# Kernel optimization log

Hardware: AMD Instinct MI355X
Metric: run time of the kernel (lower is better)

The kernel has to match this reference:

```python
import jax, jax.numpy as jnp
import numpy as np

B, T, D, R, V = 32, 14, 1024, 4, 8192


def setup_inputs() -> dict:
    key = jax.random.key(0)
    k1, k2, k3, k4, k5 = jax.random.split(key, 5)
    input_embs = jax.random.normal(k1, (B, T, D), dtype=jnp.float32)
    label_ids = jax.random.randint(k2, (B, T), 0, V)
    w_alpha = jax.random.normal(k3, (D, R), dtype=jnp.float32)
    w_beta = jax.random.normal(k4, (D, R), dtype=jnp.float32)
    w_vocab = jax.random.normal(k5, (D, V * R * R), dtype=jnp.float32)
    return {"input_embs": input_embs, "label_ids": label_ids,
            "w_alpha": w_alpha, "w_beta": w_beta, "w_vocab": w_vocab}


def _tt_params(x, w_alpha, w_beta, w_vocab):
    b, t, d = x.shape
    r = w_alpha.shape[1]
    v = w_vocab.shape[1] // (r * r)
    xf = x.reshape(-1, d)
    alpha = jax.nn.sigmoid((xf @ w_alpha).reshape(b, t, r).mean(1)) + 0.001   # (B,R)
    beta = jax.nn.sigmoid((xf @ w_beta).reshape(b, t, r).mean(1)) + 0.001     # (B,R)
    core = jax.nn.sigmoid((xf @ w_vocab).reshape(b, t, r, v, r).mean(1)) * 0.01 + 0.001  # (B,R,V,R)
    return alpha, beta, core


def _chain_matmul(init, mats):
    # init: (B,R,R); mats: (n,B,R,R) -> sequential product init @ mats[0] @ ...
    def step(carry, m):
        return jnp.einsum('bik,bkj->bij', carry, m), None
    out, _ = jax.lax.scan(step, init, mats)
    return out


def reference(input_embs, label_ids, w_alpha, w_beta, w_vocab):
    alpha, beta, core = _tt_params(input_embs, w_alpha, w_beta, w_vocab)
    b, t = label_ids.shape
    # ---- _select: gather core slices at label indices, chain-multiply ----
    sel = core[jnp.arange(b)[:, None], :, label_ids, :]   # (B,T,R,R)
    sel = jnp.swapaxes(sel, 0, 1)                         # (T,B,R,R)
    chain = _chain_matmul(sel[0], sel[1:])                # (B,R,R)
    unnorm = jnp.einsum('bi,bij,bj->b', alpha, chain, beta)
    # ---- normalization: marginalized core multiplied T extra times (T+1 factors, as in source) ----
    cm = core.sum(axis=2)                                 # (B,R,R)
    cm_rep = jnp.broadcast_to(cm, (t,) + cm.shape)        # (T,B,R,R)
    nres = _chain_matmul(cm, cm_rep)                      # (B,R,R)
    norm = jnp.einsum('bi,bij,bj->b', alpha, nres, beta)
    probs = unnorm / norm + 0.001
    loss = -jnp.log(probs)
    return loss.mean()
```

## Files before the change

kernel.cpp:

```cpp
#include <hip/hip_runtime.h>
#include <cstdint>
#include <cstddef>

#define BB 32
#define TT 14
#define DD 1024
#define RR 4
#define VV 8192
#define NCOL (VV*RR*RR)

typedef float f32x16 __attribute__((ext_vector_type(16)));
typedef short short8 __attribute__((ext_vector_type(8)));
typedef unsigned int uint;


__device__ __forceinline__ ushort bf16_rne(float f) {
    uint u = __builtin_bit_cast(uint, f);
    return (ushort)((u + 0x7FFFu + ((u >> 16) & 1u)) >> 16);
}

__global__ __launch_bounds__(256) void k_prep(const float* __restrict__ in,
                                              float* __restrict__ xb,
                                              float* __restrict__ cm) {
    int tid = blockIdx.x * 256 + threadIdx.x;
    int b = tid >> 10, d = tid & 1023;
    float s = 0.f;
    #pragma unroll
    for (int t = 0; t < TT; ++t) s += in[(b * TT + t) * DD + d];
    xb[b * DD + d] = s * (1.0f / TT);
    if (tid < BB * 16) cm[tid] = 0.f;
}

__global__ __launch_bounds__(64) void k_xfrag(const float* __restrict__ xb,
                                              uint4* __restrict__ xfrag) {
    int s = blockIdx.x;
    int l = threadIdx.x;
    int b = l & 31;
    int kb = s * 16 + (l >> 5) * 8;
    uint u[4];
    #pragma unroll
    for (int p = 0; p < 4; ++p) {
        ushort h0 = bf16_rne(xb[b * DD + kb + 2 * p]);
        ushort h1 = bf16_rne(xb[b * DD + kb + 2 * p + 1]);
        u[p] = (uint)h0 | ((uint)h1 << 16);
    }
    xfrag[(s << 6) + l] = make_uint4(u[0], u[1], u[2], u[3]);
}

__global__ __launch_bounds__(256) void k_ab(const float* __restrict__ xb,
                                            const float* __restrict__ wa,
                                            const float* __restrict__ wb,
                                            float* __restrict__ alpha,
                                            float* __restrict__ beta) {
    int wid  = (blockIdx.x * 256 + threadIdx.x) >> 6;
    int lane = threadIdx.x & 63;
    int b = wid >> 3, r = (wid >> 1) & 3, s = wid & 1;
    const float* wm = s ? wb : wa;
    float p = 0.f;
    #pragma unroll
    for (int k = 0; k < 16; ++k) {
        int d = lane + 64 * k;
        p += xb[b * DD + d] * wm[d * RR + r];
    }
    #pragma unroll
    for (int m = 1; m < 64; m <<= 1) p += __shfl_xor(p, m);
    if (lane == 0) {
        float v = 1.0f / (1.0f + __expf(-p)) + 0.001f;
        (s ? beta : alpha)[b * RR + r] = v;
    }
}

#define LOADW(DST, STEP)                                                      \
    _Pragma("unroll")                                                         \
    for (int j = 0; j < 8; ++j)                                               \
        DST[j] = __builtin_nontemporal_load(                                  \
            wp + (size_t)((STEP) * 16 + j) * NCOL);

__device__ __forceinline__ short8 pack_bf16x8(const float* w) {
    uint u[4];
    #pragma unroll
    for (int p = 0; p < 4; ++p) {
        ushort h0 = bf16_rne(w[2 * p]);
        ushort h1 = bf16_rne(w[2 * p + 1]);
        u[p] = (uint)h0 | ((uint)h1 << 16);
    }
    return __builtin_bit_cast(short8, make_uint4(u[0], u[1], u[2], u[3]));
}

__global__ __launch_bounds__(256) void k_core(const float* __restrict__ wv,
                                              const uint4* __restrict__ xfrag,
                                              const int*   __restrict__ lab,
                                              float* __restrict__ cm,
                                              float* __restrict__ sel) {
    const int tid  = threadIdx.x;
    const int lane = tid & 63;
    const int wvid = tid >> 6;
    const int n0   = blockIdx.x * 128 + wvid * 32;
    const int n    = n0 + (lane & 31);
    const int ii   = n >> 15;
    const int jj   = n & 3;
    const int vv   = (n >> 2) & (VV - 1);

    __shared__ int   lds_lab[BB * TT];
    __shared__ float cm_blk[BB][4];

    for (int idx = tid; idx < BB * TT; idx += 256) lds_lab[idx] = lab[idx];
    if (tid < BB * 4) ((float*)cm_blk)[tid] = 0.f;
    __syncthreads();

    const float* wp = wv + (size_t)((lane >> 5) * 8) * NCOL + n;

    f32x16 acc;
    #pragma unroll
    for (int q = 0; q < 16; ++q) acc[q] = 0.f;

    float wrA[8], wrB[8];
    uint4 axA, axB;
    LOADW(wrA, 0);
    axA = xfrag[lane];

    #pragma unroll 1
    for (int s = 0; s < 64; s += 2) {
        LOADW(wrB, s + 1);
        axB = xfrag[((s + 1) << 6) + lane];
        acc = __builtin_amdgcn_mfma_f32_32x32x16_bf16(
                  __builtin_bit_cast(short8, axA), pack_bf16x8(wrA), acc, 0, 0, 0);
        if (s + 2 < 64) {
            LOADW(wrA, s + 2);
            axA = xfrag[((s + 2) << 6) + lane];
        }
        acc = __builtin_amdgcn_mfma_f32_32x32x16_bf16(
                  __builtin_bit_cast(short8, axB), pack_bf16x8(wrB), acc, 0, 0, 0);
    }

    #pragma unroll
    for (int r = 0; r < 16; ++r) {
        float c = 0.01f / (1.0f + __expf(-acc[r])) + 0.001f;
        const int b = (r & 3) + 8 * (r >> 2) + 4 * (lane >> 5);
        float sred = c;
        sred += __shfl_xor(sred, 4);
        sred += __shfl_xor(sred, 8);
        sred += __shfl_xor(sred, 16);
        if ((lane & 31) < 4) atomicAdd(&cm_blk[b][lane & 3], sred);
        #pragma unroll
        for (int t = 0; t < TT; ++t)
            if (lds_lab[b * TT + t] == vv)
                sel[(b * TT + t) * 16 + (ii << 2) + jj] = c;
    }
    __syncthreads();
    if (tid < BB * 4) {
        int b = tid >> 2, j = tid & 3;
        atomicAdd(&cm[b * 16 + (ii << 2) + j], ((float*)cm_blk)[tid]);
    }
}

__global__ __launch_bounds__(64) void k_final(const float* __restrict__ cm,
                                              const float* __restrict__ sel,
                                              const float* __restrict__ alpha,
                                              const float* __restrict__ beta,
                                              float* __restrict__ out) {
    __shared__ float ls[BB];
    int b = threadIdx.x;
    if (b < BB) {
        float ch[16], tmp[16];
        #pragma unroll
        for (int q = 0; q < 16; ++q) ch[q] = sel[(b * TT + 0) * 16 + q];
        for (int t = 1; t < TT; ++t) {
            const float* m = &sel[(b * TT + t) * 16];
            #pragma unroll
            for (int i2 = 0; i2 < 4; ++i2)
                #pragma unroll
                for (int j2 = 0; j2 < 4; ++j2) {
                    float s = 0.f;
                    #pragma unroll
                    for (int k = 0; k < 4; ++k) s += ch[i2*4+k] * m[k*4+j2];
                    tmp[i2*4+j2] = s;
                }
            #pragma unroll
            for (int q = 0; q < 16; ++q) ch[q] = tmp[q];
        }

        float M[16], P[16];
        #pragma unroll
        for (int q = 0; q < 16; ++q) { M[q] = cm[b*16+q]; P[q] = M[q]; }
        for (int t = 0; t < TT; ++t) {
            #pragma unroll
            for (int i2 = 0; i2 < 4; ++i2)
                #pragma unroll
                for (int j2 = 0; j2 < 4; ++j2) {
                    float s = 0.f;
                    #pragma unroll
                    for (int k = 0; k < 4; ++k) s += P[i2*4+k] * M[k*4+j2];
                    tmp[i2*4+j2] = s;
                }
            #pragma unroll
            for (int q = 0; q < 16; ++q) P[q] = tmp[q];
        }

        float a[4], be[4];
        #pragma unroll
        for (int r = 0; r < 4; ++r) { a[r] = alpha[b*4+r]; be[r] = beta[b*4+r]; }
        float un = 0.f, no = 0.f;
        #pragma unroll
        for (int i2 = 0; i2 < 4; ++i2)
            #pragma unroll
            for (int j2 = 0; j2 < 4; ++j2) {
                un += a[i2] * ch[i2*4+j2] * be[j2];
                no += a[i2] * P [i2*4+j2] * be[j2];
            }
        float prob = un / no + 0.001f;
        ls[b] = -logf(prob);
    }
    __syncthreads();
    if (threadIdx.x == 0) {
        float s = 0.f;
        for (int q = 0; q < BB; ++q) s += ls[q];
        out[0] = s / BB;
    }
}

extern "C" void kernel_launch(void* const* d_in, const int* in_sizes, int n_in,
                              void* d_out, int out_size, void* d_ws, size_t ws_size,
                              hipStream_t stream) {
    const float* in_embs = (const float*)d_in[0];
    const int*   lab     = (const int*)  d_in[1];
    const float* wa      = (const float*)d_in[2];
    const float* wb      = (const float*)d_in[3];
    const float* wv      = (const float*)d_in[4];

    float* ws    = (float*)d_ws;
    float* xb    = ws;
    float* cm    = ws + 32768;
    float* sel   = ws + 33280;
    float* alpha = ws + 40448;
    float* beta  = ws + 40576;
    uint4* xfrag = (uint4*)(ws + 40704);

    k_prep <<<128,  256, 0, stream>>>(in_embs, xb, cm);
    k_xfrag<<<64,   64,  0, stream>>>(xb, xfrag);
    k_ab   <<<64,   256, 0, stream>>>(xb, wa, wb, alpha, beta);
    k_core <<<1024, 256, 0, stream>>>(wv, xfrag, lab, cm, sel);
    k_final<<<1,    64,  0, stream>>>(cm, sel, alpha, beta, (float*)d_out);
}
```

Baseline: 128.0 us.

## Fuse prep kernels, truncate to bf16 via perm, deepen weight prefetch

Merges the mean-pooling, bf16 fragment packing and alpha/beta projection kernels into one per-batch kernel that keeps the pooled row in LDS, cutting two launches and a global round trip. The bf16 conversion now truncates with a single byte-permute instead of round-to-nearest-even, which is cheaper but slightly changes numerics. The core GEMM loop now keeps four k-steps of weight loads in flight instead of two, which hides more memory latency at the cost of more registers.

```diff
diff --git a/kernel.cpp b/kernel.cpp
--- a/kernel.cpp
+++ b/kernel.cpp
@@ -10,63 +10,73 @@
 #define NCOL (VV*RR*RR)
 
 typedef float f32x16 __attribute__((ext_vector_type(16)));
+typedef float f4 __attribute__((ext_vector_type(4)));
 typedef short short8 __attribute__((ext_vector_type(8)));
 typedef unsigned int uint;
 
 
-__device__ __forceinline__ ushort bf16_rne(float f) {
-    uint u = __builtin_bit_cast(uint, f);
-    return (ushort)((u + 0x7FFFu + ((u >> 16) & 1u)) >> 16);
-}
-
-__global__ __launch_bounds__(256) void k_prep(const float* __restrict__ in,
-                                              float* __restrict__ xb,
-                                              float* __restrict__ cm) {
-    int tid = blockIdx.x * 256 + threadIdx.x;
-    int b = tid >> 10, d = tid & 1023;
-    float s = 0.f;
+__device__ __forceinline__ uint pack2(float a, float b) {
+    return __builtin_amdgcn_perm(__builtin_bit_cast(uint, b),
+                                 __builtin_bit_cast(uint, a), 0x07060302u);
+}
+
+__device__ __forceinline__ short8 packw(const float* w) {
+    uint4 u = make_uint4(pack2(w[0], w[1]), pack2(w[2], w[3]),
+                         pack2(w[4], w[5]), pack2(w[6], w[7]));
+    return __builtin_bit_cast(short8, u);
+}
+
+__global__ __launch_bounds__(256) void k_prep_all(const float* __restrict__ in,
+                                                  const float* __restrict__ wa,
+                                                  const float* __restrict__ wb,
+                                                  ushort* __restrict__ xfrag_us,
+                                                  float* __restrict__ alpha,
+                                                  float* __restrict__ beta,
+                                                  float* __restrict__ cm) {
+    __shared__ float xl[DD];
+    const int b   = blockIdx.x;
+    const int tid = threadIdx.x;
+    const int d0  = tid * 4;
+
+    f4 s4 = (f4){0.f, 0.f, 0.f, 0.f};
     #pragma unroll
-    for (int t = 0; t < TT; ++t) s += in[(b * TT + t) * DD + d];
-    xb[b * DD + d] = s * (1.0f / TT);
-    if (tid < BB * 16) cm[tid] = 0.f;
-}
-
-__global__ __launch_bounds__(64) void k_xfrag(const float* __restrict__ xb,
-                                              uint4* __restrict__ xfrag) {
-    int s = blockIdx.x;
-    int l = threadIdx.x;
-    int b = l & 31;
-    int kb = s * 16 + (l >> 5) * 8;
-    uint u[4];
-    #pragma unroll
-    for (int p = 0; p < 4; ++p) {
-        ushort h0 = bf16_rne(xb[b * DD + kb + 2 * p]);
-        ushort h1 = bf16_rne(xb[b * DD + kb + 2 * p + 1]);
-        u[p] = (uint)h0 | ((uint)h1 << 16);
-    }
-    xfrag[(s << 6) + l] = make_uint4(u[0], u[1], u[2], u[3]);
-}
-
-__global__ __launch_bounds__(256) void k_ab(const float* __restrict__ xb,
-                                            const float* __restrict__ wa,
-                                            const float* __restrict__ wb,
-                                            float* __restrict__ alpha,
-                                            float* __restrict__ beta) {
-    int wid  = (blockIdx.x * 256 + threadIdx.x) >> 6;
-    int lane = threadIdx.x & 63;
-    int b = wid >> 3, r = (wid >> 1) & 3, s = wid & 1;
-    const float* wm = s ? wb : wa;
-    float p = 0.f;
-    #pragma unroll
-    for (int k = 0; k < 16; ++k) {
-        int d = lane + 64 * k;
-        p += xb[b * DD + d] * wm[d * RR + r];
-    }
-    #pragma unroll
-    for (int m = 1; m < 64; m <<= 1) p += __shfl_xor(p, m);
-    if (lane == 0) {
-        float v = 1.0f / (1.0f + __expf(-p)) + 0.001f;
-        (s ? beta : alpha)[b * RR + r] = v;
+    for (int t = 0; t < TT; ++t) {
+        f4 v = *reinterpret_cast<const f4*>(&in[((b * TT + t) << 10) + d0]);
+        s4 += v;
+    }
+    s4 *= (1.0f / TT);
+    *reinterpret_cast<f4*>(&xl[d0]) = s4;
+
+    if (b == 0) { cm[tid] = 0.f; cm[tid + 256] = 0.f; }
+
+    {
+        const int s  = d0 >> 4;
+        const int h  = (d0 >> 3) & 1;
+        const int j0 = d0 & 7;
+        uint2 u;
+        u.x = pack2(s4.x, s4.y);
+        u.y = pack2(s4.z, s4.w);
+        *reinterpret_cast<uint2*>(&xfrag_us[((s * 64 + b + 32 * h) << 3) + j0]) = u;
+    }
+
+    __syncthreads();
+
+    const int wave = tid >> 6, lane = tid & 63;
+    for (int p = wave; p < 8; p += 4) {
+        const int r = p >> 1, sf = p & 1;
+        const float* wm = sf ? wb : wa;
+        float acc = 0.f;
+        #pragma unroll
+        for (int k = 0; k < 16; ++k) {
+            int d = lane + 64 * k;
+            acc += xl[d] * wm[d * RR + r];
+        }
+        #pragma unroll
+        for (int m = 1; m < 64; m <<= 1) acc += __shfl_xor(acc, m);
+        if (lane == 0) {
+            float v = 1.0f / (1.0f + __expf(-acc)) + 0.001f;
+            (sf ? beta : alpha)[b * RR + r] = v;
+        }
     }
 }
 
@@ -75,17 +85,6 @@
     for (int j = 0; j < 8; ++j)                                               \
         DST[j] = __builtin_nontemporal_load(                                  \
             wp + (size_t)((STEP) * 16 + j) * NCOL);
-
-__device__ __forceinline__ short8 pack_bf16x8(const float* w) {
-    uint u[4];
-    #pragma unroll
-    for (int p = 0; p < 4; ++p) {
-        ushort h0 = bf16_rne(w[2 * p]);
-        ushort h1 = bf16_rne(w[2 * p + 1]);
-        u[p] = (uint)h0 | ((uint)h1 << 16);
-    }
-    return __builtin_bit_cast(short8, make_uint4(u[0], u[1], u[2], u[3]));
-}
 
 __global__ __launch_bounds__(256) void k_core(const float* __restrict__ wv,
                                               const uint4* __restrict__ xfrag,
@@ -114,23 +113,27 @@
     #pragma unroll
     for (int q = 0; q < 16; ++q) acc[q] = 0.f;
 
-    float wrA[8], wrB[8];
-    uint4 axA, axB;
-    LOADW(wrA, 0);
-    axA = xfrag[lane];
+    float w0[8], w1[8], w2[8], w3[8];
+    uint4 ax0, ax1, ax2, ax3;
+    LOADW(w0, 0); ax0 = xfrag[lane];
+    LOADW(w1, 1); ax1 = xfrag[64 + lane];
 
     #pragma unroll 1
-    for (int s = 0; s < 64; s += 2) {
-        LOADW(wrB, s + 1);
-        axB = xfrag[((s + 1) << 6) + lane];
-        acc = __builtin_amdgcn_mfma_f32_32x32x16_bf16(
-                  __builtin_bit_cast(short8, axA), pack_bf16x8(wrA), acc, 0, 0, 0);
-        if (s + 2 < 64) {
-            LOADW(wrA, s + 2);
-            axA = xfrag[((s + 2) << 6) + lane];
-        }
-        acc = __builtin_amdgcn_mfma_f32_32x32x16_bf16(
-                  __builtin_bit_cast(short8, axB), pack_bf16x8(wrB), acc, 0, 0, 0);
+    for (int s = 0; s < 64; s += 4) {
+        LOADW(w2, s + 2); ax2 = xfrag[((s + 2) << 6) + lane];
+        LOADW(w3, s + 3); ax3 = xfrag[((s + 3) << 6) + lane];
+        acc = __builtin_amdgcn_mfma_f32_32x32x16_bf16(
+                  __builtin_bit_cast(short8, ax0), packw(w0), acc, 0, 0, 0);
+        acc = __builtin_amdgcn_mfma_f32_32x32x16_bf16(
+                  __builtin_bit_cast(short8, ax1), packw(w1), acc, 0, 0, 0);
+        if (s + 4 < 64) {
+            LOADW(w0, s + 4); ax0 = xfrag[((s + 4) << 6) + lane];
+            LOADW(w1, s + 5); ax1 = xfrag[((s + 5) << 6) + lane];
+        }
+        acc = __builtin_amdgcn_mfma_f32_32x32x16_bf16(
+                  __builtin_bit_cast(short8, ax2), packw(w2), acc, 0, 0, 0);
+        acc = __builtin_amdgcn_mfma_f32_32x32x16_bf16(
+                  __builtin_bit_cast(short8, ax3), packw(w3), acc, 0, 0, 0);
     }
 
     #pragma unroll
@@ -229,16 +232,14 @@
     const float* wv      = (const float*)d_in[4];
 
     float* ws    = (float*)d_ws;
-    float* xb    = ws;
-    float* cm    = ws + 32768;
-    float* sel   = ws + 33280;
-    float* alpha = ws + 40448;
-    float* beta  = ws + 40576;
-    uint4* xfrag = (uint4*)(ws + 40704);
-
-    k_prep <<<128,  256, 0, stream>>>(in_embs, xb, cm);
-    k_xfrag<<<64,   64,  0, stream>>>(xb, xfrag);
-    k_ab   <<<64,   256, 0, stream>>>(xb, wa, wb, alpha, beta);
-    k_core <<<1024, 256, 0, stream>>>(wv, xfrag, lab, cm, sel);
-    k_final<<<1,    64,  0, stream>>>(cm, sel, alpha, beta, (float*)d_out);
-}
+    float* cm    = ws;
+    float* sel   = ws + 512;
+    float* alpha = ws + 7680;
+    float* beta  = ws + 7808;
+    uint4* xfrag = (uint4*)(ws + 7936);
+
+    k_prep_all<<<32,   256, 0, stream>>>(in_embs, wa, wb, (ushort*)xfrag,
+                                         alpha, beta, cm);
+    k_core    <<<1024, 256, 0, stream>>>(wv, xfrag, lab, cm, sel);
+    k_final   <<<1,    64,  0, stream>>>(cm, sel, alpha, beta, (float*)d_out);
+}
```

Measured after the change: 115.8 us. -9.5%, faster.
